# Kernel tuning notes

Hardware: AMD Instinct MI355X
Metric: run time of the kernel (lower is better)

Reference implementation:

```python
import jax, jax.numpy as jnp
import numpy as np

HIDDEN = 1024
N_HEAD = 16
N_KV_HEAD = 4
HEAD_DIM = HIDDEN // N_HEAD  # 64


def setup_inputs() -> dict:
    key = jax.random.key(0)
    ks = jax.random.split(key, 9)
    s = 0.02
    kv_dim = N_KV_HEAD * HEAD_DIM
    return {
        "X": jax.random.normal(ks[0], (2, 2048, HIDDEN), dtype=jnp.float32),
        "Wq": jax.random.normal(ks[1], (HIDDEN, HIDDEN), dtype=jnp.float32) * s,
        "bq": jnp.zeros((HIDDEN,), dtype=jnp.float32),
        "Wk": jax.random.normal(ks[2], (HIDDEN, kv_dim), dtype=jnp.float32) * s,
        "bk": jnp.zeros((kv_dim,), dtype=jnp.float32),
        "Wv": jax.random.normal(ks[3], (HIDDEN, kv_dim), dtype=jnp.float32) * s,
        "bv": jnp.zeros((kv_dim,), dtype=jnp.float32),
        "Wo": jax.random.normal(ks[4], (HIDDEN, HIDDEN), dtype=jnp.float32) * s,
        "bo": jnp.zeros((HIDDEN,), dtype=jnp.float32),
    }


def reference(X, Wq, bq, Wk, bk, Wv, bv, Wo, bo):
    B, S, _ = X.shape
    rep = N_HEAD // N_KV_HEAD
    # projections
    q = (X @ Wq + bq).reshape(B, S, N_HEAD, HEAD_DIM).transpose(0, 2, 1, 3)      # [B,H,S,D]
    k = (X @ Wk + bk).reshape(B, S, N_KV_HEAD, HEAD_DIM).transpose(0, 2, 1, 3)   # [B,Hkv,S,D]
    v = (X @ Wv + bv).reshape(B, S, N_KV_HEAD, HEAD_DIM).transpose(0, 2, 1, 3)
    # repeat_interleave KV heads to full head count (faithful to original)
    k = jnp.repeat(k, rep, axis=1)  # [B,H,S,D]
    v = jnp.repeat(v, rep, axis=1)
    scale = 1.0 / jnp.sqrt(jnp.float32(HEAD_DIM))
    scores = jnp.einsum("bhqd,bhkd->bhqk", q, k) * scale  # [B,H,S,S]
    weights = jax.nn.softmax(scores, axis=-1)
    out = jnp.einsum("bhqk,bhkd->bhqd", weights, v)       # [B,H,S,D]
    out = out.transpose(0, 2, 1, 3).reshape(B, S, HIDDEN)
    return out @ Wo + bo
```

## Files before the change

kernel.cpp:

```cpp
#include <hip/hip_runtime.h>
#include <hip/hip_bf16.h>

#define HIDDEN 1024
#define NHEAD 16
#define NKV 4
#define HDIM 64
#define KVDIM 256
#define SEQ 2048
#define BATCH 2
#define NQKV 1536

typedef __attribute__((ext_vector_type(4)))  float f32x4;
typedef __attribute__((ext_vector_type(16))) float f32x16;
typedef __attribute__((ext_vector_type(8)))  short s16x8;
typedef __attribute__((ext_vector_type(4)))  short s16x4;

#if defined(__has_builtin)
#if __has_builtin(__builtin_amdgcn_exp2f)
#define EXP2F(x) __builtin_amdgcn_exp2f(x)
#else
#define EXP2F(x) exp2f(x)
#endif
#else
#define EXP2F(x) exp2f(x)
#endif

static __device__ __forceinline__ ushort f2bf(float f) {
    union { __hip_bfloat16 b; ushort u; } cv; cv.b = __float2bfloat16(f); return cv.u;
}
static __device__ __forceinline__ unsigned pack_rh2(float a, float b) {
    unsigned ua = __float_as_uint(a) + 0x8000u;
    unsigned ub = __float_as_uint(b) + 0x8000u;
    return (ua >> 16) | (ub & 0xFFFF0000u);
}
static __device__ __forceinline__ void async16(const void* g, void* l) {
    __builtin_amdgcn_global_load_lds((__attribute__((address_space(1))) void*)g,
                                     (__attribute__((address_space(3))) void*)l, 16, 0, 0);
}

__global__ __launch_bounds__(256)
void cvt_x(const float* __restrict__ in, ushort* __restrict__ out)
{
    int i = blockIdx.x * 256 + threadIdx.x;
    float4 v = ((const float4*)in)[i];
    ushort4 o;
    o.x = f2bf(v.x); o.y = f2bf(v.y); o.z = f2bf(v.z); o.w = f2bf(v.w);
    ((ushort4*)out)[i] = o;
}

__global__ __launch_bounds__(256)
void wtrans_qkv(const float* __restrict__ Wq, const float* __restrict__ Wk,
                const float* __restrict__ Wv, ushort* __restrict__ T)
{
    __shared__ float Tl[64][65];
    const int bx = blockIdx.x, k0 = blockIdx.y * 64;
    const float* W; int N, n0, roff;
    if (bx < 16)      { W = Wq; N = 1024; n0 = bx * 64;        roff = 0; }
    else if (bx < 20) { W = Wk; N = 256;  n0 = (bx - 16) * 64; roff = 1024; }
    else              { W = Wv; N = 256;  n0 = (bx - 20) * 64; roff = 1280; }
    const int tid = threadIdx.x;
#pragma unroll
    for (int it = 0; it < 4; it++) {
        int idx = tid + it * 256;
        int kk = idx >> 4, n4 = (idx & 15) * 4;
        float4 v = *(const float4*)(W + (size_t)(k0 + kk) * N + n0 + n4);
        Tl[kk][n4 + 0] = v.x; Tl[kk][n4 + 1] = v.y;
        Tl[kk][n4 + 2] = v.z; Tl[kk][n4 + 3] = v.w;
    }
    __syncthreads();
#pragma unroll
    for (int it = 0; it < 4; it++) {
        int idx = tid + it * 256;
        int n = idx >> 4, k4 = (idx & 15) * 4;
        ushort4 h4;
        h4.x = f2bf(Tl[k4 + 0][n]); h4.y = f2bf(Tl[k4 + 1][n]);
        h4.z = f2bf(Tl[k4 + 2][n]); h4.w = f2bf(Tl[k4 + 3][n]);
        *(ushort4*)(T + (size_t)(roff + n0 + n) * HIDDEN + k0 + k4) = h4;
    }
}

__global__ __launch_bounds__(256)
void wtrans_one(const float* __restrict__ W, ushort* __restrict__ T,
                int N, int K)
{
    __shared__ float Tl[64][65];
    const int n0 = blockIdx.x * 64, k0 = blockIdx.y * 64;
    const int tid = threadIdx.x;
#pragma unroll
    for (int it = 0; it < 4; it++) {
        int idx = tid + it * 256;
        int kk = idx >> 4, n4 = (idx & 15) * 4;
        float4 v = *(const float4*)(W + (size_t)(k0 + kk) * N + n0 + n4);
        Tl[kk][n4 + 0] = v.x; Tl[kk][n4 + 1] = v.y;
        Tl[kk][n4 + 2] = v.z; Tl[kk][n4 + 3] = v.w;
    }
    __syncthreads();
#pragma unroll
    for (int it = 0; it < 4; it++) {
        int idx = tid + it * 256;
        int n = idx >> 4, k4 = (idx & 15) * 4;
        ushort4 h4;
        h4.x = f2bf(Tl[k4 + 0][n]); h4.y = f2bf(Tl[k4 + 1][n]);
        h4.z = f2bf(Tl[k4 + 2][n]); h4.w = f2bf(Tl[k4 + 3][n]);
        *(ushort4*)(T + (size_t)(n0 + n) * K + k0 + k4) = h4;
    }
}

template <int MODE>
__global__ __launch_bounds__(256)
void gemm_bf(const ushort* __restrict__ A, const ushort* __restrict__ Bt,
             const float* __restrict__ b0, const float* __restrict__ b1,
             const float* __restrict__ b2, void* __restrict__ Cout,
             int M, int N, int K)
{
    __shared__ __align__(16) ushort Ah[64 * 32];
    __shared__ __align__(16) ushort Bh[128 * 32];

    const int tid = threadIdx.x;
    const int lane = tid & 63, wv = tid >> 6;
    const int wr = wv >> 1, wc = wv & 1;
    const int m = lane & 15, c = lane >> 4;
    const int row0 = blockIdx.y * 64, col0 = blockIdx.x * 128;

    const ushort* gA = A + (size_t)(row0 + (tid >> 2)) * K + (tid & 3) * 8;
    const int ldsA = tid * 8;
    const ushort* gB[2]; int ldsB[2];
#pragma unroll
    for (int it = 0; it < 2; it++) {
        int idx = it * 256 + tid;
        gB[it] = Bt + (size_t)(col0 + (idx >> 2)) * K + (idx & 3) * 8;
        ldsB[it] = idx * 8;
    }

    f32x4 acc[2][4];
#pragma unroll
    for (int t = 0; t < 2; t++)
#pragma unroll
        for (int u = 0; u < 4; u++) acc[t][u] = (f32x4){0.f, 0.f, 0.f, 0.f};

    for (int k0 = 0; k0 < K; k0 += 32) {
        __syncthreads();
        async16(gA + k0, Ah + ldsA);
#pragma unroll
        for (int it = 0; it < 2; it++) async16(gB[it] + k0, Bh + ldsB[it]);
        __syncthreads();

        s16x8 ah[2], bh[4];
#pragma unroll
        for (int t = 0; t < 2; t++)
            ah[t] = *(const s16x8*)&Ah[(wr * 32 + t * 16 + m) * 32 + c * 8];
#pragma unroll
        for (int u = 0; u < 4; u++)
            bh[u] = *(const s16x8*)&Bh[(wc * 64 + u * 16 + m) * 32 + c * 8];
#pragma unroll
        for (int t = 0; t < 2; t++)
#pragma unroll
            for (int u = 0; u < 4; u++)
                acc[t][u] = __builtin_amdgcn_mfma_f32_16x16x32_bf16(ah[t], bh[u], acc[t][u], 0, 0, 0);
    }

    const int orow = row0 + wr * 32 + 4 * c;
    const int ocol = col0 + wc * 64 + m;
    if (MODE == 0) {
        ushort* Cb = (ushort*)Cout;
#pragma unroll
        for (int u = 0; u < 4; u++) {
            int n = ocol + 16 * u;
            float bias, scl;
            if (n < 1024)      { bias = b0[n];        scl = 0.18033688f; }
            else if (n < 1280) { bias = b1[n - 1024]; scl = 1.0f; }
            else               { bias = b2[n - 1280]; scl = 1.0f; }
#pragma unroll
            for (int t = 0; t < 2; t++)
#pragma unroll
                for (int r = 0; r < 4; r++)
                    Cb[(size_t)(orow + 16 * t + r) * N + n] = f2bf((acc[t][u][r] + bias) * scl);
        }
    } else {
        float* Cf = (float*)Cout;
#pragma unroll
        for (int u = 0; u < 4; u++) {
            int n = ocol + 16 * u;
            float bias = b0[n];
#pragma unroll
            for (int t = 0; t < 2; t++)
#pragma unroll
                for (int r = 0; r < 4; r++)
                    Cf[(size_t)(orow + 16 * t + r) * N + n] = acc[t][u][r] + bias;
        }
    }
}

__global__ __launch_bounds__(256)
void kvpack(const ushort* __restrict__ QKV, ushort* __restrict__ Kf,
            ushort* __restrict__ Vf)
{
    __shared__ __align__(16) ushort Kt[64][72];
    __shared__ __align__(16) ushort Vt[64][72];
    const int kt = blockIdx.x, hk = blockIdx.y, b = blockIdx.z;
    const int tid = threadIdx.x;

#pragma unroll
    for (int it = 0; it < 2; it++) {
        int idx = tid + it * 256;
        int r = idx >> 3, c8 = (idx & 7) * 8;
        const ushort* src = QKV + (size_t)(b * SEQ + kt * 64 + r) * NQKV + hk * HDIM + c8;
        *(s16x8*)&Kt[r][c8] = *(const s16x8*)(src + 1024);
        *(s16x8*)&Vt[r][c8] = *(const s16x8*)(src + 1280);
    }
    __syncthreads();

#pragma unroll
    for (int it = 0; it < 2; it++) {
        int idx = tid + it * 256;
        int t32 = idx >> 8, kc = (idx >> 6) & 3, lane = idx & 63;
        int n32 = lane & 31, h5 = lane >> 5;
        s16x8 fr = *(const s16x8*)&Kt[t32 * 32 + n32][kc * 16 + h5 * 8];
        size_t flat = ((size_t)(((b * NKV + hk) * 64 + kt * 2 + t32) * 4 + kc) * 64 + lane) * 8;
        *(s16x8*)(Kf + flat) = fr;
    }
#pragma unroll
    for (int it = 0; it < 2; it++) {
        int idx = tid + it * 256;
        int kcdn = idx >> 6, lane = idx & 63;
        int kc = kcdn >> 1, dn = kcdn & 1;
        int n32 = lane & 31, h5 = lane >> 5;
        s16x8 fr;
#pragma unroll
        for (int j = 0; j < 8; j++)
            fr[j] = (short)Vt[kc * 16 + h5 * 8 + j][dn * 32 + n32];
        size_t flat = ((size_t)(((b * NKV + hk) * 32 + kt) * 8 + kc * 2 + dn) * 64 + lane) * 8;
        *(s16x8*)(Vf + flat) = fr;
    }
}

__global__ __launch_bounds__(512, 2)
void attn_mfma7(const ushort* __restrict__ QKV, const ushort* __restrict__ Kf,
                const ushort* __restrict__ Vf, ushort* __restrict__ Chi)
{
    __shared__ __align__(16) ushort Ps[8][32][68];
    float* OLb = (float*)&Ps[0][0][0];
    float* LLb = (float*)((char*)&Ps[0][0][0] + 33024);

    const int tid = threadIdx.x, w = tid >> 6, lane = tid & 63;
    const int g = w >> 2, ws_ = w & 3;
    const int n32 = lane & 31, h5 = lane >> 5;
    const int h = blockIdx.y, b = blockIdx.z, hk = h >> 2;
    const int q0 = blockIdx.x * 64 + g * 32;

    const ushort* qrow = QKV + (size_t)(b * SEQ + q0 + n32) * NQKV + h * HDIM + h5 * 8;
    s16x8 aq[4];
#pragma unroll
    for (int kc = 0; kc < 4; kc++) aq[kc] = *(const s16x8*)(qrow + kc * 16);

    f32x16 accO[2], accl;
#pragma unroll
    for (int j = 0; j < 16; j++) { accO[0][j] = 0.f; accO[1][j] = 0.f; accl[j] = 0.f; }

    s16x8 ones;
#pragma unroll
    for (int j = 0; j < 8; j++) ones[j] = (short)0x3F80;

    const ushort* kf0 = Kf + (size_t)(b * NKV + hk) * (64 * 4 * 64 * 8) + (size_t)lane * 8;
    const ushort* vf0 = Vf + (size_t)(b * NKV + hk) * (32 * 8 * 64 * 8) + (size_t)lane * 8;

    s16x8 kreg[8], vreg[8];

#define LOAD_K(kt_) do {                                                      \
    _Pragma("unroll")                                                         \
    for (int kn = 0; kn < 2; kn++)                                            \
        _Pragma("unroll")                                                     \
        for (int kc = 0; kc < 4; kc++)                                        \
            kreg[kn * 4 + kc] =                                               \
                *(const s16x8*)(kf0 + (size_t)(((kt_) * 2 + kn) * 4 + kc) * 512); \
} while (0)

#define LOAD_V(kt_) do {                                                      \
    _Pragma("unroll")                                                         \
    for (int kc = 0; kc < 4; kc++)                                            \
        _Pragma("unroll")                                                     \
        for (int dn = 0; dn < 2; dn++)                                        \
            vreg[kc * 2 + dn] =                                               \
                *(const s16x8*)(vf0 + (size_t)((kt_) * 8 + kc * 2 + dn) * 512); \
} while (0)

#define QK_EXP_STORE() do {                                                   \
    _Pragma("unroll")                                                         \
    for (int kn = 0; kn < 2; kn++) {                                          \
        f32x16 S;                                                             \
        _Pragma("unroll")                                                     \
        for (int j = 0; j < 16; j++) S[j] = 0.f;                              \
        _Pragma("unroll")                                                     \
        for (int kc = 0; kc < 4; kc++)                                        \
            S = __builtin_amdgcn_mfma_f32_32x32x16_bf16(kreg[kn * 4 + kc],    \
                    aq[kc], S, 0, 0, 0);                                      \
        float p[16];                                                          \
        _Pragma("unroll")                                                     \
        for (int reg = 0; reg < 16; reg++) p[reg] = EXP2F(S[reg]);            \
        _Pragma("unroll")                                                     \
        for (int t = 0; t < 4; t++) {                                         \
            uint2 pk;                                                         \
            pk.x = pack_rh2(p[4 * t + 0], p[4 * t + 1]);                      \
            pk.y = pack_rh2(p[4 * t + 2], p[4 * t + 3]);                      \
            *(uint2*)&Ps[w][n32][kn * 32 + 8 * t + 4 * h5] = pk;              \
        }                                                                     \
    }                                                                         \
} while (0)

#define PV_STEP() do {                                                        \
    s16x8 pa[4];                                                              \
    _Pragma("unroll")                                                         \
    for (int kc = 0; kc < 4; kc++) {                                          \
        s16x4 lo4 = *(const s16x4*)&Ps[w][n32][kc * 16 + h5 * 8];             \
        s16x4 hi4 = *(const s16x4*)&Ps[w][n32][kc * 16 + h5 * 8 + 4];         \
        pa[kc] = __builtin_shufflevector(lo4, hi4, 0, 1, 2, 3, 4, 5, 6, 7);   \
    }                                                                         \
    _Pragma("unroll")                                                         \
    for (int kc = 0; kc < 4; kc++) {                                          \
        accl = __builtin_amdgcn_mfma_f32_32x32x16_bf16(pa[kc], ones, accl, 0, 0, 0); \
        _Pragma("unroll")                                                     \
        for (int dn = 0; dn < 2; dn++)                                        \
            accO[dn] = __builtin_amdgcn_mfma_f32_32x32x16_bf16(pa[kc],        \
                           vreg[kc * 2 + dn], accO[dn], 0, 0, 0);             \
    }                                                                         \
} while (0)

    LOAD_K(ws_);
    QK_EXP_STORE();

    for (int i = 1; i < 8; i++) {
        const int ktc = ws_ + 4 * i;
        LOAD_V(ktc - 4);
        LOAD_K(ktc);
        PV_STEP();
        QK_EXP_STORE();
    }

    LOAD_V(ws_ + 28);
    PV_STEP();

#undef LOAD_K
#undef LOAD_V
#undef QK_EXP_STORE
#undef PV_STEP

    __syncthreads();

    const int qq = tid >> 4;
    const int d0 = (tid & 15) * 4;
#pragma unroll
    for (int phase = 0; phase < 2; phase++) {
        if (g == phase) {
#pragma unroll
            for (int reg = 0; reg < 16; reg++) {
                int q = (reg & 3) + 8 * (reg >> 2) + 4 * h5;
                OLb[(ws_ * 32 + q) * 64 + n32]      = accO[0][reg];
                OLb[(ws_ * 32 + q) * 64 + 32 + n32] = accO[1][reg];
                if (n32 == 0) LLb[ws_ * 32 + q] = accl[reg];
            }
        }
        __syncthreads();
        {
            float lsum = LLb[qq] + LLb[32 + qq] + LLb[64 + qq] + LLb[96 + qq];
            float inv = 1.f / lsum;
            ushort4 hs;
            float o0 = (OLb[(0 * 32 + qq) * 64 + d0 + 0] + OLb[(1 * 32 + qq) * 64 + d0 + 0] +
                        OLb[(2 * 32 + qq) * 64 + d0 + 0] + OLb[(3 * 32 + qq) * 64 + d0 + 0]) * inv;
            float o1 = (OLb[(0 * 32 + qq) * 64 + d0 + 1] + OLb[(1 * 32 + qq) * 64 + d0 + 1] +
                        OLb[(2 * 32 + qq) * 64 + d0 + 1] + OLb[(3 * 32 + qq) * 64 + d0 + 1]) * inv;
            float o2 = (OLb[(0 * 32 + qq) * 64 + d0 + 2] + OLb[(1 * 32 + qq) * 64 + d0 + 2] +
                        OLb[(2 * 32 + qq) * 64 + d0 + 2] + OLb[(3 * 32 + qq) * 64 + d0 + 2]) * inv;
            float o3 = (OLb[(0 * 32 + qq) * 64 + d0 + 3] + OLb[(1 * 32 + qq) * 64 + d0 + 3] +
                        OLb[(2 * 32 + qq) * 64 + d0 + 3] + OLb[(3 * 32 + qq) * 64 + d0 + 3]) * inv;
            hs.x = f2bf(o0); hs.y = f2bf(o1); hs.z = f2bf(o2); hs.w = f2bf(o3);
            size_t off = (size_t)(b * SEQ + blockIdx.x * 64 + phase * 32 + qq) * HIDDEN
                       + h * HDIM + d0;
            *(ushort4*)(Chi + off) = hs;
        }
        __syncthreads();
    }
}

extern "C" void kernel_launch(void* const* d_in, const int* in_sizes, int n_in,
                              void* d_out, int out_size, void* d_ws, size_t ws_size,
                              hipStream_t stream)
{
    const float* X  = (const float*)d_in[0];
    const float* Wq = (const float*)d_in[1];
    const float* bq = (const float*)d_in[2];
    const float* Wk = (const float*)d_in[3];
    const float* bk = (const float*)d_in[4];
    const float* Wv = (const float*)d_in[5];
    const float* bv = (const float*)d_in[6];
    const float* Wo = (const float*)d_in[7];
    const float* bo = (const float*)d_in[8];
    float* out = (float*)d_out;

    const int M = BATCH * SEQ;
    char* ws = (char*)d_ws;
    ushort* Xb    = (ushort*)(ws);
    ushort* Ctx   = (ushort*)(ws + (8u  << 20));
    ushort* QKVb  = (ushort*)(ws + (16u << 20));
    ushort* Wqkvt = (ushort*)(ws + (28u << 20));
    ushort* Wot   = (ushort*)(ws + (31u << 20));
    ushort* Kf    = (ushort*)(ws + (33u << 20));
    ushort* Vf    = (ushort*)(ws + (35u << 20));

    cvt_x<<<dim3(M * HIDDEN / 4 / 256), 256, 0, stream>>>(X, Xb);
    wtrans_qkv<<<dim3(24, 16), 256, 0, stream>>>(Wq, Wk, Wv, Wqkvt);
    wtrans_one<<<dim3(16, 16), 256, 0, stream>>>(Wo, Wot, 1024, HIDDEN);

    gemm_bf<0><<<dim3(NQKV / 128, M / 64), 256, 0, stream>>>(
        Xb, Wqkvt, bq, bk, bv, (void*)QKVb, M, NQKV, HIDDEN);

    kvpack<<<dim3(SEQ / 64, NKV, BATCH), 256, 0, stream>>>(QKVb, Kf, Vf);

    attn_mfma7<<<dim3(SEQ / 64, NHEAD, BATCH), 512, 0, stream>>>(QKVb, Kf, Vf, Ctx);

    gemm_bf<1><<<dim3(HIDDEN / 128, M / 64), 256, 0, stream>>>(
        Ctx, Wot, bo, nullptr, nullptr, (void*)out, M, HIDDEN, HIDDEN);
}
```

Baseline: 196.2 us.

## Merge prep kernels and double-buffer V fragments in attention loop

Folds the X conversion and both weight transposes into one prep kernel, which removes two launch overheads. In the attention kernel, the V tile is now prefetched into alternating register buffers one iteration earlier, alongside the K tile. This lets global loads of V overlap with the preceding PV and QK work. The cost is extra vector registers, which could cause spills or lower occupancy under the (512,2) launch bound.

New measurement: 189.4 us. -3.5%, faster.

```diff
diff --git a/kernel.cpp b/kernel.cpp
--- a/kernel.cpp
+++ b/kernel.cpp
@@ -39,26 +39,37 @@
 }
 
 __global__ __launch_bounds__(256)
-void cvt_x(const float* __restrict__ in, ushort* __restrict__ out)
-{
-    int i = blockIdx.x * 256 + threadIdx.x;
-    float4 v = ((const float4*)in)[i];
-    ushort4 o;
-    o.x = f2bf(v.x); o.y = f2bf(v.y); o.z = f2bf(v.z); o.w = f2bf(v.w);
-    ((ushort4*)out)[i] = o;
-}
-
-__global__ __launch_bounds__(256)
-void wtrans_qkv(const float* __restrict__ Wq, const float* __restrict__ Wk,
-                const float* __restrict__ Wv, ushort* __restrict__ T)
+void prep(const float* __restrict__ X, ushort* __restrict__ Xb,
+          const float* __restrict__ Wq, const float* __restrict__ Wk,
+          const float* __restrict__ Wv, ushort* __restrict__ Tqkv,
+          const float* __restrict__ Wo, ushort* __restrict__ Two)
 {
     __shared__ float Tl[64][65];
-    const int bx = blockIdx.x, k0 = blockIdx.y * 64;
-    const float* W; int N, n0, roff;
-    if (bx < 16)      { W = Wq; N = 1024; n0 = bx * 64;        roff = 0; }
-    else if (bx < 20) { W = Wk; N = 256;  n0 = (bx - 16) * 64; roff = 1024; }
-    else              { W = Wv; N = 256;  n0 = (bx - 20) * 64; roff = 1280; }
-    const int tid = threadIdx.x;
+    const int bid = blockIdx.x, tid = threadIdx.x;
+
+    if (bid < 4096) {
+        int i = bid * 256 + tid;
+        float4 v = ((const float4*)X)[i];
+        ushort4 o;
+        o.x = f2bf(v.x); o.y = f2bf(v.y); o.z = f2bf(v.z); o.w = f2bf(v.w);
+        ((ushort4*)Xb)[i] = o;
+        return;
+    }
+
+    const float* W; ushort* T; int N, n0, k0, roff;
+    if (bid < 4096 + 384) {
+        int wq = bid - 4096;
+        int bx = wq % 24; k0 = (wq / 24) * 64;
+        T = Tqkv;
+        if (bx < 16)      { W = Wq; N = 1024; n0 = bx * 64;        roff = 0; }
+        else if (bx < 20) { W = Wk; N = 256;  n0 = (bx - 16) * 64; roff = 1024; }
+        else              { W = Wv; N = 256;  n0 = (bx - 20) * 64; roff = 1280; }
+    } else {
+        int wo = bid - 4480;
+        int bx = wo % 16; k0 = (wo / 16) * 64;
+        W = Wo; T = Two; N = 1024; n0 = bx * 64; roff = 0;
+    }
+
 #pragma unroll
     for (int it = 0; it < 4; it++) {
         int idx = tid + it * 256;
@@ -76,33 +87,6 @@
         h4.x = f2bf(Tl[k4 + 0][n]); h4.y = f2bf(Tl[k4 + 1][n]);
         h4.z = f2bf(Tl[k4 + 2][n]); h4.w = f2bf(Tl[k4 + 3][n]);
         *(ushort4*)(T + (size_t)(roff + n0 + n) * HIDDEN + k0 + k4) = h4;
-    }
-}
-
-__global__ __launch_bounds__(256)
-void wtrans_one(const float* __restrict__ W, ushort* __restrict__ T,
-                int N, int K)
-{
-    __shared__ float Tl[64][65];
-    const int n0 = blockIdx.x * 64, k0 = blockIdx.y * 64;
-    const int tid = threadIdx.x;
-#pragma unroll
-    for (int it = 0; it < 4; it++) {
-        int idx = tid + it * 256;
-        int kk = idx >> 4, n4 = (idx & 15) * 4;
-        float4 v = *(const float4*)(W + (size_t)(k0 + kk) * N + n0 + n4);
-        Tl[kk][n4 + 0] = v.x; Tl[kk][n4 + 1] = v.y;
-        Tl[kk][n4 + 2] = v.z; Tl[kk][n4 + 3] = v.w;
-    }
-    __syncthreads();
-#pragma unroll
-    for (int it = 0; it < 4; it++) {
-        int idx = tid + it * 256;
-        int n = idx >> 4, k4 = (idx & 15) * 4;
-        ushort4 h4;
-        h4.x = f2bf(Tl[k4 + 0][n]); h4.y = f2bf(Tl[k4 + 1][n]);
-        h4.z = f2bf(Tl[k4 + 2][n]); h4.w = f2bf(Tl[k4 + 3][n]);
-        *(ushort4*)(T + (size_t)(n0 + n) * K + k0 + k4) = h4;
     }
 }
 
@@ -235,7 +219,7 @@
 }
 
 __global__ __launch_bounds__(512, 2)
-void attn_mfma7(const ushort* __restrict__ QKV, const ushort* __restrict__ Kf,
+void attn_mfma9(const ushort* __restrict__ QKV, const ushort* __restrict__ Kf,
                 const ushort* __restrict__ Vf, ushort* __restrict__ Chi)
 {
     __shared__ __align__(16) ushort Ps[8][32][68];
@@ -264,7 +248,7 @@
     const ushort* kf0 = Kf + (size_t)(b * NKV + hk) * (64 * 4 * 64 * 8) + (size_t)lane * 8;
     const ushort* vf0 = Vf + (size_t)(b * NKV + hk) * (32 * 8 * 64 * 8) + (size_t)lane * 8;
 
-    s16x8 kreg[8], vreg[8];
+    s16x8 kreg[8], vregA[8], vregB[8];
 
 #define LOAD_K(kt_) do {                                                      \
     _Pragma("unroll")                                                         \
@@ -275,12 +259,12 @@
                 *(const s16x8*)(kf0 + (size_t)(((kt_) * 2 + kn) * 4 + kc) * 512); \
 } while (0)
 
-#define LOAD_V(kt_) do {                                                      \
+#define LOAD_V(kt_, VR) do {                                                  \
     _Pragma("unroll")                                                         \
     for (int kc = 0; kc < 4; kc++)                                            \
         _Pragma("unroll")                                                     \
         for (int dn = 0; dn < 2; dn++)                                        \
-            vreg[kc * 2 + dn] =                                               \
+            VR[kc * 2 + dn] =                                                 \
                 *(const s16x8*)(vf0 + (size_t)((kt_) * 8 + kc * 2 + dn) * 512); \
 } while (0)
 
@@ -307,7 +291,7 @@
     }                                                                         \
 } while (0)
 
-#define PV_STEP() do {                                                        \
+#define PV_STEP(VR) do {                                                      \
     s16x8 pa[4];                                                              \
     _Pragma("unroll")                                                         \
     for (int kc = 0; kc < 4; kc++) {                                          \
@@ -321,23 +305,29 @@
         _Pragma("unroll")                                                     \
         for (int dn = 0; dn < 2; dn++)                                        \
             accO[dn] = __builtin_amdgcn_mfma_f32_32x32x16_bf16(pa[kc],        \
-                           vreg[kc * 2 + dn], accO[dn], 0, 0, 0);             \
+                           VR[kc * 2 + dn], accO[dn], 0, 0, 0);               \
     }                                                                         \
 } while (0)
 
     LOAD_K(ws_);
+    LOAD_V(ws_, vregA);
     QK_EXP_STORE();
 
-    for (int i = 1; i < 8; i++) {
-        const int ktc = ws_ + 4 * i;
-        LOAD_V(ktc - 4);
-        LOAD_K(ktc);
-        PV_STEP();
+#pragma unroll
+    for (int ii = 0; ii < 3; ii++) {
+        const int t1 = ws_ + 4 * (1 + 2 * ii);
+        const int t2 = ws_ + 4 * (2 + 2 * ii);
+        LOAD_K(t1); LOAD_V(t1, vregB);
+        PV_STEP(vregA);
         QK_EXP_STORE();
-    }
-
-    LOAD_V(ws_ + 28);
-    PV_STEP();
+        LOAD_K(t2); LOAD_V(t2, vregA);
+        PV_STEP(vregB);
+        QK_EXP_STORE();
+    }
+    LOAD_K(ws_ + 28); LOAD_V(ws_ + 28, vregB);
+    PV_STEP(vregA);
+    QK_EXP_STORE();
+    PV_STEP(vregB);
 
 #undef LOAD_K
 #undef LOAD_V
@@ -406,16 +396,14 @@
     ushort* Kf    = (ushort*)(ws + (33u << 20));
     ushort* Vf    = (ushort*)(ws + (35u << 20));
 
-    cvt_x<<<dim3(M * HIDDEN / 4 / 256), 256, 0, stream>>>(X, Xb);
-    wtrans_qkv<<<dim3(24, 16), 256, 0, stream>>>(Wq, Wk, Wv, Wqkvt);
-    wtrans_one<<<dim3(16, 16), 256, 0, stream>>>(Wo, Wot, 1024, HIDDEN);
+    prep<<<dim3(4736), 256, 0, stream>>>(X, Xb, Wq, Wk, Wv, Wqkvt, Wo, Wot);
 
     gemm_bf<0><<<dim3(NQKV / 128, M / 64), 256, 0, stream>>>(
         Xb, Wqkvt, bq, bk, bv, (void*)QKVb, M, NQKV, HIDDEN);
 
     kvpack<<<dim3(SEQ / 64, NKV, BATCH), 256, 0, stream>>>(QKVb, Kf, Vf);
 
-    attn_mfma7<<<dim3(SEQ / 64, NHEAD, BATCH), 512, 0, stream>>>(QKVb, Kf, Vf, Ctx);
+    attn_mfma9<<<dim3(SEQ / 64, NHEAD, BATCH), 512, 0, stream>>>(QKVb, Kf, Vf, Ctx);
 
     gemm_bf<1><<<dim3(HIDDEN / 128, M / 64), 256, 0, stream>>>(
         Ctx, Wot, bo, nullptr, nullptr, (void*)out, M, HIDDEN, HIDDEN);
```
